# Kernel optimization log

Hardware: AMD Instinct MI355X
Metric: run time of the kernel (lower is better)

## Reference

```python
import jax, jax.numpy as jnp
import numpy as np

LAYERS = 30
LAYERS_PER_STACK = 10
OUT_CH = 256
RES_CH = 64
GATE_CH = 128
SKIP_CH = 64
CIN_CH = 80
UPSAMPLE_SCALES = (10, 8)


def setup_inputs() -> dict:
    key = jax.random.key(0)
    ks = iter(jax.random.split(key, 32))
    B, T_frames = 8, 400
    T = T_frames * int(np.prod(UPSAMPLE_SCALES))  # 32000
    s = 0.05
    inp = {
        "x": jax.random.randint(next(ks), (B, T), 0, OUT_CH, dtype=jnp.int64),
        "condition": jax.random.normal(next(ks), (B, CIN_CH, T_frames), dtype=jnp.float32),
        # first 1x1 conv: one-hot(256) -> res(64)
        "first_w": jax.random.normal(next(ks), (RES_CH, OUT_CH), dtype=jnp.float32) * s,
        "first_b": jnp.zeros((RES_CH,), dtype=jnp.float32),
        # upsample conv_in (kernel_size = 2*0+1 = 1, no bias)
        "cin_w": jax.random.normal(next(ks), (CIN_CH, CIN_CH), dtype=jnp.float32) * s,
        # per-layer stacked params (30 layers)
        "conv_w": jax.random.normal(next(ks), (LAYERS, GATE_CH, RES_CH, 2), dtype=jnp.float32) * s,
        "conv_b": jnp.zeros((LAYERS, GATE_CH), dtype=jnp.float32),
        "cond_w": jax.random.normal(next(ks), (LAYERS, GATE_CH, CIN_CH), dtype=jnp.float32) * s,
        "skip_w": jax.random.normal(next(ks), (LAYERS, SKIP_CH, GATE_CH // 2), dtype=jnp.float32) * s,
        "skip_b": jnp.zeros((LAYERS, SKIP_CH), dtype=jnp.float32),
        "out_w": jax.random.normal(next(ks), (LAYERS, RES_CH, GATE_CH // 2), dtype=jnp.float32) * s,
        "out_b": jnp.zeros((LAYERS, RES_CH), dtype=jnp.float32),
        # last 1x1 convs: skip->skip, skip->out_channels
        "last1_w": jax.random.normal(next(ks), (SKIP_CH, SKIP_CH), dtype=jnp.float32) * s,
        "last1_b": jnp.zeros((SKIP_CH,), dtype=jnp.float32),
        "last2_w": jax.random.normal(next(ks), (OUT_CH, SKIP_CH), dtype=jnp.float32) * s,
        "last2_b": jnp.zeros((OUT_CH,), dtype=jnp.float32),
    }
    return inp


def _upsample(c, cin_w):
    # conv_in: 1x1 (aux_context_window=0), no bias
    c = jnp.einsum('oi,bif->bof', cin_w, c)
    for scale in UPSAMPLE_SCALES:
        # nearest upsample along time, then (1, 2s+1) averaging conv (depthwise, zero pad)
        c = jnp.repeat(c, scale, axis=2)
        kw = 2 * scale + 1
        kern = jnp.full((c.shape[1], 1, kw), 1.0 / kw, dtype=c.dtype)  # [C,1,kw]
        c = jax.lax.conv_general_dilated(
            c, kern, window_strides=(1,), padding=[(scale, scale)],
            dimension_numbers=('NCH', 'OIH', 'NCH'),
            feature_group_count=c.shape[1])
    return c  # [B, CIN_CH, T]


def _wavenet_forward(x, condition, first_w, first_b, cin_w, conv_w, conv_b,
                     cond_w, skip_w, skip_b, out_w, out_b,
                     last1_w, last1_b, last2_w, last2_b):
    B, T = x.shape
    oh = jax.nn.one_hot(x, OUT_CH, dtype=first_w.dtype)            # [B,T,256]
    h = jnp.einsum('oi,bti->bot', first_w, oh) + first_b[None, :, None]  # [B,64,T]
    c = _upsample(condition, cin_w)                                 # [B,80,T]

    skips = jnp.zeros((B, SKIP_CH, T), dtype=h.dtype)
    for l in range(LAYERS):
        d = 2 ** (l % LAYERS_PER_STACK)
        # causal dilated conv, kernel=2: tap0 sees x[t-d], tap1 sees x[t]
        h_shift = jnp.pad(h, ((0, 0), (0, 0), (d, 0)))[:, :, :T]
        g = (jnp.einsum('oi,bit->bot', conv_w[l, :, :, 0], h_shift)
             + jnp.einsum('oi,bit->bot', conv_w[l, :, :, 1], h)
             + conv_b[l][None, :, None])                            # [B,128,T]
        g = g + jnp.einsum('oi,bit->bot', cond_w[l], c)             # local conditioning
        a, b = jnp.split(g, 2, axis=1)
        z = jnp.tanh(a) * jax.nn.sigmoid(b)                         # [B,64,T]
        skips = skips + jnp.einsum('oi,bit->bot', skip_w[l], z) + skip_b[l][None, :, None]
        h = h + jnp.einsum('oi,bit->bot', out_w[l], z) + out_b[l][None, :, None]

    y = jax.nn.relu(skips)
    y = jnp.einsum('oi,bit->bot', last1_w, y) + last1_b[None, :, None]
    y = jax.nn.relu(y)
    y = jnp.einsum('oi,bit->bot', last2_w, y) + last2_b[None, :, None]
    return y  # [B,256,T] logits


def reference(x, condition, first_w, first_b, cin_w, conv_w, conv_b, cond_w,
              skip_w, skip_b, out_w, out_b, last1_w, last1_b, last2_w, last2_b):
    return _wavenet_forward(x, condition, first_w, first_b, cin_w, conv_w, conv_b,
                            cond_w, skip_w, skip_b, out_w, out_b,
                            last1_w, last1_b, last2_w, last2_b)
```

## Files before the change

### kernel.cpp

```cpp
#include <hip/hip_runtime.h>

#define NB 8
#define T 32000
#define NLAYERS 30
#define RES 64
#define GATE 128
#define SKIPC 64
#define CIN 80
#define OUTC 256
#define TF 400
#define TM 4000

#define K1 208
#define AHI_SZ 26624
#define A2SZ   8192
#define A2_OFF (2*AHI_SZ)
#define L_U16  (2*AHI_SZ + 2*A2SZ)

typedef __bf16 bf16x8 __attribute__((ext_vector_type(8)));
typedef float  f32x16 __attribute__((ext_vector_type(16)));

__device__ __forceinline__ unsigned short bf16_rtne(float x) {
    unsigned u = __float_as_uint(x);
    u += 0x7fffu + ((u >> 16) & 1u);
    return (unsigned short)(u >> 16);
}
__device__ __forceinline__ float bf16_f(unsigned short h) {
    return __uint_as_float(((unsigned)h) << 16);
}
__device__ __forceinline__ unsigned split_pack(float x) {
    unsigned short hi = bf16_rtne(x);
    unsigned short lo = bf16_rtne(x - bf16_f(hi));
    return (unsigned)hi | ((unsigned)lo << 16);
}

__global__ void pack_weights(const float* __restrict__ conv_w,
                             const float* __restrict__ cond_w,
                             const float* __restrict__ skip_w,
                             const float* __restrict__ out_w,
                             const float* __restrict__ last1_w,
                             unsigned short* __restrict__ wp16,
                             float* __restrict__ l1t) {
    int e = blockIdx.x * 256 + threadIdx.x;
    const int NW = NLAYERS * 34816;
    if (e < NW) {
        int l = e / 34816, r = e % 34816;
        float wv;
        int dst, losz;
        if (r < 26624) {
            int pr = r / K1, k = r % K1;
            int o = (pr & 1) * 64 + (pr >> 1);
            if (k < 64)       wv = conv_w[((l*GATE + o)*RES + k)*2 + 0];
            else if (k < 128) wv = conv_w[((l*GATE + o)*RES + (k-64))*2 + 1];
            else              wv = cond_w[(l*GATE + o)*CIN + (k-128)];
            int w = pr >> 5, r31 = pr & 31, kc = k >> 4, lg2 = (k >> 3) & 1, ee = k & 7;
            dst = l*L_U16 + ((w*13 + kc)*64 + lg2*32 + r31)*8 + ee;
            losz = AHI_SZ;
        } else {
            int r2 = r - 26624;
            int row = r2 >> 6, k = r2 & 63;
            wv = (row < 64) ? skip_w[(l*64 + row)*64 + k]
                            : out_w[(l*64 + (row-64))*64 + k];
            int w = row >> 5, r31 = row & 31, kc = k >> 4, lg2 = (k >> 3) & 1, ee = k & 7;
            dst = l*L_U16 + A2_OFF + ((w*4 + kc)*64 + lg2*32 + r31)*8 + ee;
            losz = A2SZ;
        }
        unsigned short hi = bf16_rtne(wv);
        wp16[dst] = hi;
        wp16[dst + losz] = bf16_rtne(wv - bf16_f(hi));
    } else if (e < NW + 4096) {
        int r = e - NW;
        int i = r >> 6, o = r & 63;
        l1t[r] = last1_w[o * 64 + i];
    }
}

__global__ void first_conv(const int* __restrict__ x, const float* __restrict__ fw,
                           const float* __restrict__ fb, unsigned* __restrict__ h) {
    int tid = blockIdx.x * 256 + threadIdx.x;
    int b = tid / T, t = tid - b * T;
    int idx = x[tid];
    int base = (b * RES) * T + t;
    for (int o = 0; o < RES; ++o)
        h[base + o * T] = split_pack(fw[o * OUTC + idx] + fb[o]);
}

__global__ void cond_in(const float* __restrict__ cond, const float* __restrict__ cw,
                        float* __restrict__ c1) {
    int tid = blockIdx.x * blockDim.x + threadIdx.x;
    if (tid >= NB * TF) return;
    int b = tid / TF, t = tid - b * TF;
    float in[CIN];
#pragma unroll
    for (int i = 0; i < CIN; ++i) in[i] = cond[(b * CIN + i) * TF + t];
    for (int o = 0; o < CIN; ++o) {
        float acc = 0.f;
#pragma unroll
        for (int i = 0; i < CIN; ++i) acc += cw[o * CIN + i] * in[i];
        c1[(b * CIN + o) * TF + t] = acc;
    }
}

__global__ void up1(const float* __restrict__ src, float* __restrict__ dst) {
    int tid = blockIdx.x * 256 + threadIdx.x;
    int t = tid % TM, rc = tid / TM;
    const float* s = src + rc * TF;
    float acc = 0.f;
#pragma unroll
    for (int k = -10; k <= 10; ++k) {
        int j = t + k;
        if (j >= 0 && j < TM) acc += s[j / 10];
    }
    dst[tid] = acc * (1.f / 21.f);
}

__global__ void up2(const float* __restrict__ src, unsigned* __restrict__ dst) {
    int tid = blockIdx.x * 256 + threadIdx.x;
    int t = tid % T, rc = tid / T;
    const float* s = src + rc * TM;
    float acc = 0.f;
#pragma unroll
    for (int k = -8; k <= 8; ++k) {
        int j = t + k;
        if (j >= 0 && j < T) acc += s[j >> 3];
    }
    dst[tid] = split_pack(acc * (1.f / 17.f));
}

__global__ __launch_bounds__(512, 4)
void layer_k(const unsigned* __restrict__ h_in, unsigned* __restrict__ h_out,
             float* __restrict__ skips, const unsigned* __restrict__ c,
             const unsigned short* __restrict__ wp16,
             const float* __restrict__ conv_b, const float* __restrict__ skip_b,
             const float* __restrict__ out_b,
             int l, int d, int first) {
    __shared__ __align__(16) unsigned short Bh[13*2*64*8];
    __shared__ __align__(16) unsigned short Bl[13*2*64*8];
    __shared__ __align__(16) unsigned short Zh[4*2*64*8];
    __shared__ __align__(16) unsigned short Zl[4*2*64*8];

    int tid = threadIdx.x;
    int blk = blockIdx.x;
    int b = blk / (T/64);
    int t0 = (blk % (T/64)) * 64;
    int w8 = tid >> 6, lane = tid & 63;
    int wr = w8 >> 1, wc = w8 & 1;
    int l31 = lane & 31, lg = lane >> 5;

    {
        int col = lane;
        int tcol = t0 + col;
        const unsigned* hb = h_in + b * (RES * T);
        const unsigned* cb = c + b * (CIN * T);
        for (int kk = w8; kk < 52; kk += 8) {
            int k = kk * 4;
            unsigned v0, v1, v2, v3;
            if (k < 64) {
                int ts = tcol - d;
                bool ok = ts >= 0;
                v0 = ok ? hb[(k+0)*T + ts] : 0u;
                v1 = ok ? hb[(k+1)*T + ts] : 0u;
                v2 = ok ? hb[(k+2)*T + ts] : 0u;
                v3 = ok ? hb[(k+3)*T + ts] : 0u;
            } else if (k < 128) {
                v0 = hb[(k-64)*T + tcol];
                v1 = hb[(k-63)*T + tcol];
                v2 = hb[(k-62)*T + tcol];
                v3 = hb[(k-61)*T + tcol];
            } else {
                v0 = cb[(k-128)*T + tcol];
                v1 = cb[(k-127)*T + tcol];
                v2 = cb[(k-126)*T + tcol];
                v3 = cb[(k-125)*T + tcol];
            }
            uint2 whi = make_uint2((v0 & 0xffffu) | (v1 << 16),
                                   (v2 & 0xffffu) | (v3 << 16));
            uint2 wlo = make_uint2((v0 >> 16) | (v1 & 0xffff0000u),
                                   (v2 >> 16) | (v3 & 0xffff0000u));
            int off = ((k >> 4)*2 + (col >> 5))*512 + ((col & 31) + (((k >> 3) & 1) << 5))*8 + (k & 7);
            *(uint2*)(Bh + off) = whi;
            *(uint2*)(Bl + off) = wlo;
        }
    }
    __syncthreads();

    const unsigned short* wA = wp16 + l * L_U16;

    f32x16 acc;
#pragma unroll
    for (int i = 0; i < 16; ++i) acc[i] = 0.f;
    {
        const bf16x8* BhF = (const bf16x8*)Bh;
        const bf16x8* BlF = (const bf16x8*)Bl;
        const unsigned short* aG = wA + (wr*13*64 + lane)*8;
#pragma unroll
        for (int kc = 0; kc < 13; ++kc) {
            bf16x8 ah = *(const bf16x8*)(aG + kc*512);
            bf16x8 al = *(const bf16x8*)(aG + AHI_SZ + kc*512);
            bf16x8 bh = BhF[(kc*2 + wc)*64 + lane];
            bf16x8 bl = BlF[(kc*2 + wc)*64 + lane];
            acc = __builtin_amdgcn_mfma_f32_32x32x16_bf16(ah, bh, acc, 0, 0, 0);
            acc = __builtin_amdgcn_mfma_f32_32x32x16_bf16(ah, bl, acc, 0, 0, 0);
            acc = __builtin_amdgcn_mfma_f32_32x32x16_bf16(al, bh, acc, 0, 0, 0);
        }
    }

    {
        const float* cbl = conv_b + l * GATE;
        unsigned* Zh32 = (unsigned*)Zh;
        unsigned* Zl32 = (unsigned*)Zl;
#pragma unroll
        for (int q = 0; q < 8; q += 2) {
            float z2[2];
#pragma unroll
            for (int s = 0; s < 2; ++s) {
                int qq = q + s;
                int jl = 4*(qq >> 1) + 2*lg + (qq & 1);
                int zr = 16*wr + jl;
                float a  = acc[2*qq]     + cbl[zr];
                float bb = acc[2*qq + 1] + cbl[64 + zr];
                a  = fminf(fmaxf(a, -15.f), 15.f);
                bb = fminf(fmaxf(bb, -30.f), 30.f);
                float e2 = __expf(2.f * a);
                float th = (e2 - 1.f) / (e2 + 1.f);
                float sg = 1.f / (1.f + __expf(-bb));
                z2[s] = th * sg;
            }
            unsigned short h0 = bf16_rtne(z2[0]);
            unsigned short h1 = bf16_rtne(z2[1]);
            unsigned short o0 = bf16_rtne(z2[0] - bf16_f(h0));
            unsigned short o1 = bf16_rtne(z2[1] - bf16_f(h1));
            int jl0 = 4*(q >> 1) + 2*lg;
            int zr = 16*wr + jl0;
            int off = ((zr >> 4)*2 + wc)*512 + (l31 + (((zr >> 3) & 1) << 5))*8 + (zr & 7);
            Zh32[off >> 1] = (unsigned)h0 | ((unsigned)h1 << 16);
            Zl32[off >> 1] = (unsigned)o0 | ((unsigned)o1 << 16);
        }
    }
    __syncthreads();

    f32x16 s0;
#pragma unroll
    for (int i = 0; i < 16; ++i) s0[i] = 0.f;
    {
        const bf16x8* ZhF = (const bf16x8*)Zh;
        const bf16x8* ZlF = (const bf16x8*)Zl;
        const unsigned short* aG2 = wA + A2_OFF + (wr*4*64 + lane)*8;
#pragma unroll
        for (int kc = 0; kc < 4; ++kc) {
            bf16x8 ah = *(const bf16x8*)(aG2 + kc*512);
            bf16x8 al = *(const bf16x8*)(aG2 + A2SZ + kc*512);
            bf16x8 bh = ZhF[(kc*2 + wc)*64 + lane];
            bf16x8 bl = ZlF[(kc*2 + wc)*64 + lane];
            s0 = __builtin_amdgcn_mfma_f32_32x32x16_bf16(ah, bh, s0, 0, 0, 0);
            s0 = __builtin_amdgcn_mfma_f32_32x32x16_bf16(ah, bl, s0, 0, 0, 0);
            s0 = __builtin_amdgcn_mfma_f32_32x32x16_bf16(al, bh, s0, 0, 0, 0);
        }
    }

    int tcol0 = t0 + wc*32 + l31;
    if (wr < 2) {
        float* sp = skips + (b * SKIPC) * T + tcol0;
        const float* sbl = skip_b + l * SKIPC;
#pragma unroll
        for (int reg = 0; reg < 16; ++reg) {
            int row = 32*wr + (reg & 3) + 8*(reg >> 2) + 4*lg;
            int idx = row * T;
            float v = s0[reg] + sbl[row];
            if (!first) v += sp[idx];
            sp[idx] = v;
        }
    } else {
        unsigned* ho = h_out + b * (RES * T) + tcol0;
        const unsigned* hp = h_in + b * (RES * T) + tcol0;
        const float* obl = out_b + l * RES;
#pragma unroll
        for (int reg = 0; reg < 16; ++reg) {
            int row = 32*(wr - 2) + (reg & 3) + 8*(reg >> 2) + 4*lg;
            int idx = row * T;
            unsigned hv = hp[idx];
            float hf = bf16_f((unsigned short)(hv & 0xffffu)) +
                       bf16_f((unsigned short)(hv >> 16));
            ho[idx] = split_pack(hf + s0[reg] + obl[row]);
        }
    }
}

__global__ __launch_bounds__(256, 2)
void final_k(const float* __restrict__ skips, const float* __restrict__ l1T,
             const float* __restrict__ b1, const float* __restrict__ l2w,
             const float* __restrict__ b2, float* __restrict__ out) {
    int tid = blockIdx.x * 256 + threadIdx.x;
    int b = tid / T, t = tid - b * T;
    int sbase = (b * SKIPC) * T + t;
    float y1[64];
#pragma unroll
    for (int o = 0; o < 64; ++o) y1[o] = b1[o];
    for (int i = 0; i < 64; ++i) {
        float s = fmaxf(skips[sbase + i * T], 0.f);
        const float* w = l1T + i * 64;
#pragma unroll
        for (int o = 0; o < 64; ++o) y1[o] += w[o] * s;
    }
#pragma unroll
    for (int o = 0; o < 64; ++o) y1[o] = fmaxf(y1[o], 0.f);
    int obase = (b * OUTC) * T + t;
    for (int o2 = 0; o2 < OUTC; ++o2) {
        const float* w = l2w + o2 * 64;
        float acc = b2[o2];
#pragma unroll
        for (int i = 0; i < 64; ++i) acc += w[i] * y1[i];
        out[obase + o2 * T] = acc;
    }
}

extern "C" void kernel_launch(void* const* d_in, const int* in_sizes, int n_in,
                              void* d_out, int out_size, void* d_ws, size_t ws_size,
                              hipStream_t stream) {
    const int*   x       = (const int*)  d_in[0];
    const float* cond    = (const float*)d_in[1];
    const float* first_w = (const float*)d_in[2];
    const float* first_b = (const float*)d_in[3];
    const float* cin_w   = (const float*)d_in[4];
    const float* conv_w  = (const float*)d_in[5];
    const float* conv_b  = (const float*)d_in[6];
    const float* cond_w  = (const float*)d_in[7];
    const float* skip_w  = (const float*)d_in[8];
    const float* skip_b  = (const float*)d_in[9];
    const float* out_w   = (const float*)d_in[10];
    const float* out_b   = (const float*)d_in[11];
    const float* last1_w = (const float*)d_in[12];
    const float* last1_b = (const float*)d_in[13];
    const float* last2_w = (const float*)d_in[14];
    const float* last2_b = (const float*)d_in[15];
    float* out = (float*)d_out;

    float* ws = (float*)d_ws;
    float* l1t = ws;
    unsigned short* wp16 = (unsigned short*)(ws + 4096);
    float* skips = ws + 4096 + (NLAYERS * L_U16) / 2;
    unsigned* c = (unsigned*)(skips + NB * SKIPC * T);

    unsigned* hA = (unsigned*)out;
    unsigned* hB = hA + NB * RES * T;
    float* c2 = (float*)(hB + NB * RES * T);
    float* c1 = c2 + NB * CIN * TM;

    pack_weights<<<4096, 256, 0, stream>>>(conv_w, cond_w, skip_w, out_w,
                                           last1_w, wp16, l1t);
    first_conv<<<(NB * T) / 256, 256, 0, stream>>>(x, first_w, first_b, hA);
    cond_in<<<(NB * TF + 255) / 256, 256, 0, stream>>>(cond, cin_w, c1);
    up1<<<(NB * CIN * TM) / 256, 256, 0, stream>>>(c1, c2);
    up2<<<(NB * CIN * T) / 256, 256, 0, stream>>>(c2, c);

    for (int l = 0; l < NLAYERS; ++l) {
        int d = 1 << (l % 10);
        const unsigned* h_in = (l & 1) ? hB : hA;
        unsigned*       h_out = (l & 1) ? hA : hB;
        layer_k<<<NB * (T / 64), 512, 0, stream>>>(h_in, h_out, skips, c, wp16,
                                                   conv_b, skip_b, out_b,
                                                   l, d, (l == 0) ? 1 : 0);
    }
    final_k<<<(NB * T) / 256, 256, 0, stream>>>(skips, l1t, last1_b, last2_w, last2_b, out);
}
```

Measured before the change: 6.243 ms.

## Move final 1x1 conv head to split-bf16 MFMA with packed weights

```diff
diff --git a/kernel.cpp b/kernel.cpp
--- a/kernel.cpp
+++ b/kernel.cpp
@@ -16,6 +16,10 @@
 #define A2SZ   8192
 #define A2_OFF (2*AHI_SZ)
 #define L_U16  (2*AHI_SZ + 2*A2SZ)
+#define FIN_OFF (NLAYERS * L_U16)
+#define L1P_SZ 4096
+#define L2P_SZ 16384
+#define WP16_TOTAL (FIN_OFF + 2*L1P_SZ + 2*L2P_SZ)
 
 typedef __bf16 bf16x8 __attribute__((ext_vector_type(8)));
 typedef float  f32x16 __attribute__((ext_vector_type(16)));
@@ -39,14 +43,16 @@
                              const float* __restrict__ skip_w,
                              const float* __restrict__ out_w,
                              const float* __restrict__ last1_w,
-                             unsigned short* __restrict__ wp16,
-                             float* __restrict__ l1t) {
+                             const float* __restrict__ last2_w,
+                             unsigned short* __restrict__ wp16) {
     int e = blockIdx.x * 256 + threadIdx.x;
     const int NW = NLAYERS * 34816;
+    const int TOTAL = NW + L1P_SZ + L2P_SZ;
+    if (e >= TOTAL) return;
+    float wv;
+    int dst, losz;
     if (e < NW) {
         int l = e / 34816, r = e % 34816;
-        float wv;
-        int dst, losz;
         if (r < 26624) {
             int pr = r / K1, k = r % K1;
             int o = (pr & 1) * 64 + (pr >> 1);
@@ -65,14 +71,24 @@
             dst = l*L_U16 + A2_OFF + ((w*4 + kc)*64 + lg2*32 + r31)*8 + ee;
             losz = A2SZ;
         }
-        unsigned short hi = bf16_rtne(wv);
-        wp16[dst] = hi;
-        wp16[dst + losz] = bf16_rtne(wv - bf16_f(hi));
-    } else if (e < NW + 4096) {
+    } else if (e < NW + L1P_SZ) {
         int r = e - NW;
-        int i = r >> 6, o = r & 63;
-        l1t[r] = last1_w[o * 64 + i];
-    }
+        int row = r >> 6, k = r & 63;
+        wv = last1_w[row * 64 + k];
+        int rw = row >> 5, kc = k >> 4;
+        dst = FIN_OFF + ((rw*4 + kc)*64 + ((k>>3)&1)*32 + (row&31))*8 + (k&7);
+        losz = L1P_SZ;
+    } else {
+        int r = e - NW - L1P_SZ;
+        int row = r >> 6, k = r & 63;
+        wv = last2_w[row * 64 + k];
+        int rw = row >> 5, kc = k >> 4;
+        dst = FIN_OFF + 2*L1P_SZ + ((rw*4 + kc)*64 + ((k>>3)&1)*32 + (row&31))*8 + (k&7);
+        losz = L2P_SZ;
+    }
+    unsigned short hi = bf16_rtne(wv);
+    wp16[dst] = hi;
+    wp16[dst + losz] = bf16_rtne(wv - bf16_f(hi));
 }
 
 __global__ void first_conv(const int* __restrict__ x, const float* __restrict__ fw,
@@ -286,32 +302,118 @@
     }
 }
 
+__device__ __forceinline__ void store_block(float* __restrict__ op,
+                                            const float* __restrict__ b2,
+                                            const f32x16& S, int rowb, int ntc, int lg) {
+#pragma unroll
+    for (int reg = 0; reg < 16; ++reg) {
+        int row = rowb + (reg & 3) + 8*(reg >> 2) + 4*lg;
+        op[row * T + ntc*32] = S[reg] + b2[row];
+    }
+}
+
 __global__ __launch_bounds__(256, 2)
-void final_k(const float* __restrict__ skips, const float* __restrict__ l1T,
-             const float* __restrict__ b1, const float* __restrict__ l2w,
-             const float* __restrict__ b2, float* __restrict__ out) {
-    int tid = blockIdx.x * 256 + threadIdx.x;
-    int b = tid / T, t = tid - b * T;
-    int sbase = (b * SKIPC) * T + t;
-    float y1[64];
-#pragma unroll
-    for (int o = 0; o < 64; ++o) y1[o] = b1[o];
-    for (int i = 0; i < 64; ++i) {
-        float s = fmaxf(skips[sbase + i * T], 0.f);
-        const float* w = l1T + i * 64;
-#pragma unroll
-        for (int o = 0; o < 64; ++o) y1[o] += w[o] * s;
-    }
-#pragma unroll
-    for (int o = 0; o < 64; ++o) y1[o] = fmaxf(y1[o], 0.f);
-    int obase = (b * OUTC) * T + t;
-    for (int o2 = 0; o2 < OUTC; ++o2) {
-        const float* w = l2w + o2 * 64;
-        float acc = b2[o2];
-#pragma unroll
-        for (int i = 0; i < 64; ++i) acc += w[i] * y1[i];
-        out[obase + o2 * T] = acc;
-    }
+void final_k(const float* __restrict__ skips, const unsigned short* __restrict__ wp16,
+             const float* __restrict__ b1, const float* __restrict__ b2,
+             float* __restrict__ out) {
+    __shared__ __align__(16) unsigned short Sh[4*2*64*8];
+    __shared__ __align__(16) unsigned short Sl[4*2*64*8];
+    __shared__ __align__(16) unsigned short Yh[4*2*64*8];
+    __shared__ __align__(16) unsigned short Yl[4*2*64*8];
+    int tid = threadIdx.x, blk = blockIdx.x;
+    int b = blk / (T/64), t0 = (blk % (T/64)) * 64;
+    int w = tid >> 6, lane = tid & 63;
+    int l31 = lane & 31, lg = lane >> 5;
+
+    {
+        const float* sp = skips + (b * SKIPC) * T + t0 + lane;
+        unsigned* Sh32 = (unsigned*)Sh;
+        unsigned* Sl32 = (unsigned*)Sl;
+#pragma unroll
+        for (int kk = 0; kk < 16; kk += 2) {
+            int k = w*16 + kk;
+            float v0 = fmaxf(sp[k*T], 0.f);
+            float v1 = fmaxf(sp[(k+1)*T], 0.f);
+            unsigned p0 = split_pack(v0), p1 = split_pack(v1);
+            int off = ((k>>4)*2 + (lane>>5))*512 + ((lane&31) + (((k>>3)&1)<<5))*8 + (k&7);
+            Sh32[off >> 1] = (p0 & 0xffffu) | (p1 << 16);
+            Sl32[off >> 1] = (p0 >> 16) | (p1 & 0xffff0000u);
+        }
+    }
+    __syncthreads();
+
+    int rw = w & 1, nt1 = w >> 1;
+    f32x16 y;
+#pragma unroll
+    for (int i = 0; i < 16; ++i) y[i] = 0.f;
+    {
+        const bf16x8* ShF = (const bf16x8*)Sh;
+        const bf16x8* SlF = (const bf16x8*)Sl;
+        const unsigned short* aG = wp16 + FIN_OFF + (rw*4*64 + lane)*8;
+#pragma unroll
+        for (int kc = 0; kc < 4; ++kc) {
+            bf16x8 ah = *(const bf16x8*)(aG + kc*512);
+            bf16x8 al = *(const bf16x8*)(aG + L1P_SZ + kc*512);
+            bf16x8 bh = ShF[(kc*2 + nt1)*64 + lane];
+            bf16x8 bl = SlF[(kc*2 + nt1)*64 + lane];
+            y = __builtin_amdgcn_mfma_f32_32x32x16_bf16(ah, bh, y, 0, 0, 0);
+            y = __builtin_amdgcn_mfma_f32_32x32x16_bf16(ah, bl, y, 0, 0, 0);
+            y = __builtin_amdgcn_mfma_f32_32x32x16_bf16(al, bh, y, 0, 0, 0);
+        }
+    }
+    {
+        unsigned* Yh32 = (unsigned*)Yh;
+        unsigned* Yl32 = (unsigned*)Yl;
+#pragma unroll
+        for (int reg = 0; reg < 16; reg += 2) {
+            int row0 = 32*rw + (reg & 3) + 8*(reg >> 2) + 4*lg;
+            float v0 = fmaxf(y[reg]     + b1[row0],     0.f);
+            float v1 = fmaxf(y[reg + 1] + b1[row0 + 1], 0.f);
+            unsigned p0 = split_pack(v0), p1 = split_pack(v1);
+            int off = ((row0>>4)*2 + nt1)*512 + (l31 + (((row0>>3)&1)<<5))*8 + (row0&7);
+            Yh32[off >> 1] = (p0 & 0xffffu) | (p1 << 16);
+            Yl32[off >> 1] = (p0 >> 16) | (p1 & 0xffff0000u);
+        }
+    }
+    __syncthreads();
+
+    f32x16 o00, o01, o10, o11;
+#pragma unroll
+    for (int i = 0; i < 16; ++i) { o00[i] = 0.f; o01[i] = 0.f; o10[i] = 0.f; o11[i] = 0.f; }
+    {
+        const bf16x8* YhF = (const bf16x8*)Yh;
+        const bf16x8* YlF = (const bf16x8*)Yl;
+        const unsigned short* aG2 = wp16 + FIN_OFF + 2*L1P_SZ;
+        int rb0 = 2*w, rb1 = 2*w + 1;
+#pragma unroll
+        for (int kc = 0; kc < 4; ++kc) {
+            bf16x8 a0h = *(const bf16x8*)(aG2 + ((rb0*4 + kc)*64 + lane)*8);
+            bf16x8 a0l = *(const bf16x8*)(aG2 + L2P_SZ + ((rb0*4 + kc)*64 + lane)*8);
+            bf16x8 a1h = *(const bf16x8*)(aG2 + ((rb1*4 + kc)*64 + lane)*8);
+            bf16x8 a1l = *(const bf16x8*)(aG2 + L2P_SZ + ((rb1*4 + kc)*64 + lane)*8);
+            bf16x8 bh0 = YhF[(kc*2 + 0)*64 + lane];
+            bf16x8 bh1 = YhF[(kc*2 + 1)*64 + lane];
+            bf16x8 bl0 = YlF[(kc*2 + 0)*64 + lane];
+            bf16x8 bl1 = YlF[(kc*2 + 1)*64 + lane];
+            o00 = __builtin_amdgcn_mfma_f32_32x32x16_bf16(a0h, bh0, o00, 0, 0, 0);
+            o00 = __builtin_amdgcn_mfma_f32_32x32x16_bf16(a0h, bl0, o00, 0, 0, 0);
+            o00 = __builtin_amdgcn_mfma_f32_32x32x16_bf16(a0l, bh0, o00, 0, 0, 0);
+            o01 = __builtin_amdgcn_mfma_f32_32x32x16_bf16(a0h, bh1, o01, 0, 0, 0);
+            o01 = __builtin_amdgcn_mfma_f32_32x32x16_bf16(a0h, bl1, o01, 0, 0, 0);
+            o01 = __builtin_amdgcn_mfma_f32_32x32x16_bf16(a0l, bh1, o01, 0, 0, 0);
+            o10 = __builtin_amdgcn_mfma_f32_32x32x16_bf16(a1h, bh0, o10, 0, 0, 0);
+            o10 = __builtin_amdgcn_mfma_f32_32x32x16_bf16(a1h, bl0, o10, 0, 0, 0);
+            o10 = __builtin_amdgcn_mfma_f32_32x32x16_bf16(a1l, bh0, o10, 0, 0, 0);
+            o11 = __builtin_amdgcn_mfma_f32_32x32x16_bf16(a1h, bh1, o11, 0, 0, 0);
+            o11 = __builtin_amdgcn_mfma_f32_32x32x16_bf16(a1h, bl1, o11, 0, 0, 0);
+            o11 = __builtin_amdgcn_mfma_f32_32x32x16_bf16(a1l, bh1, o11, 0, 0, 0);
+        }
+    }
+    float* op = out + (b * OUTC) * T + t0 + l31;
+    store_block(op, b2, o00, 64*w,      0, lg);
+    store_block(op, b2, o01, 64*w,      1, lg);
+    store_block(op, b2, o10, 64*w + 32, 0, lg);
+    store_block(op, b2, o11, 64*w + 32, 1, lg);
 }
 
 extern "C" void kernel_launch(void* const* d_in, const int* in_sizes, int n_in,
@@ -335,10 +437,8 @@
     const float* last2_b = (const float*)d_in[15];
     float* out = (float*)d_out;
 
-    float* ws = (float*)d_ws;
-    float* l1t = ws;
-    unsigned short* wp16 = (unsigned short*)(ws + 4096);
-    float* skips = ws + 4096 + (NLAYERS * L_U16) / 2;
+    unsigned short* wp16 = (unsigned short*)d_ws;
+    float* skips = (float*)d_ws + WP16_TOTAL / 2;
     unsigned* c = (unsigned*)(skips + NB * SKIPC * T);
 
     unsigned* hA = (unsigned*)out;
@@ -346,8 +446,8 @@
     float* c2 = (float*)(hB + NB * RES * T);
     float* c1 = c2 + NB * CIN * TM;
 
-    pack_weights<<<4096, 256, 0, stream>>>(conv_w, cond_w, skip_w, out_w,
-                                           last1_w, wp16, l1t);
+    pack_weights<<<4160, 256, 0, stream>>>(conv_w, cond_w, skip_w, out_w,
+                                           last1_w, last2_w, wp16);
     first_conv<<<(NB * T) / 256, 256, 0, stream>>>(x, first_w, first_b, hA);
     cond_in<<<(NB * TF + 255) / 256, 256, 0, stream>>>(cond, cin_w, c1);
     up1<<<(NB * CIN * TM) / 256, 256, 0, stream>>>(c1, c2);
@@ -361,5 +461,5 @@
                                                    conv_b, skip_b, out_b,
                                                    l, d, (l == 0) ? 1 : 0);
     }
-    final_k<<<(NB * T) / 256, 256, 0, stream>>>(skips, l1t, last1_b, last2_w, last2_b, out);
-}
+    final_k<<<NB * (T / 64), 256, 0, stream>>>(skips, wp16, last1_b, last2_b, out);
+}
```

After: 5.834 ms. -6.6%, faster.
